# Performance work log

Hardware: AMD Instinct MI355X
Metric: run time of the kernel (lower is better)

Reference implementation:

```python
import jax, jax.numpy as jnp
import numpy as np

NUM_HEADS = 4
SPATIAL_DS = 2
EPS = 1e-5


def setup_inputs() -> dict:
    key = jax.random.key(0)
    ks = jax.random.split(key, 6)
    B, C, H, W = 8, 256, 64, 64
    hd = C // NUM_HEADS
    return {
        "x": jax.random.normal(ks[0], (B, C, H, W), jnp.float32),
        "gn_w": jnp.ones((C,), jnp.float32),
        "gn_b": jnp.zeros((C,), jnp.float32),
        "wq": jax.random.normal(ks[1], (C, C), jnp.float32) * (C ** -0.5),
        "wk": jax.random.normal(ks[2], (hd, C), jnp.float32) * (C ** -0.5),
        "wv": jax.random.normal(ks[3], (hd, C), jnp.float32) * (C ** -0.5),
        "wo": jax.random.normal(ks[4], (C, C), jnp.float32) * (C ** -0.5),
        "gamma": jnp.full((C,), 1e-4, jnp.float32),
    }


def reference(x, gn_w, gn_b, wq, wk, wv, wo, gamma):
    B, C, H, W = x.shape
    hd = C // NUM_HEADS
    scale = hd ** -0.5
    ds = SPATIAL_DS

    # GroupNorm with 1 group: normalize over (C,H,W) per sample, per-channel affine
    mu = jnp.mean(x, axis=(1, 2, 3), keepdims=True)
    var = jnp.var(x, axis=(1, 2, 3), keepdims=True)
    xn = (x - mu) * jax.lax.rsqrt(var + EPS)
    xn = xn * gn_w[None, :, None, None] + gn_b[None, :, None, None]

    # Q projection (1x1 conv == channel matmul): (B, heads, N, hd)
    q = jnp.einsum('oc,bchw->bohw', wq, xn).reshape(B, NUM_HEADS, hd, H * W)
    q = jnp.swapaxes(q, 2, 3)  # (B, h, N, hd)

    # AvgPool2d(ds, ds) on normalized input for K/V
    Hd, Wd = H // ds, W // ds
    x_ds = xn.reshape(B, C, Hd, ds, Wd, ds).mean(axis=(3, 5))

    k = jnp.einsum('oc,bchw->bohw', wk, x_ds).reshape(B, hd, Hd * Wd)
    k = jnp.swapaxes(k, 1, 2)  # (B, M, hd) single shared head
    v = jnp.einsum('oc,bchw->bohw', wv, x_ds).reshape(B, hd, Hd * Wd)
    v = jnp.swapaxes(v, 1, 2)  # (B, M, hd)

    # Multi-query attention: queries per-head, shared K/V
    attn = jnp.einsum('bhnd,bmd->bhnm', q, k) * scale
    attn = jax.nn.softmax(attn, axis=-1)
    out = jnp.einsum('bhnm,bmd->bhnd', attn, v)  # (B, h, N, hd)

    out = jnp.swapaxes(out, 2, 3).reshape(B, C, H, W)
    out = jnp.einsum('oc,bchw->bohw', wo, out)

    return x + out * gamma[None, :, None, None]
```

## Files before the change

### kernel.cpp

```cpp
#include <hip/hip_runtime.h>


#define CNT_INV (1.0f/1048576.0f)
#define EPSV 1e-5f
#define QSCALE 0.18033688f

#define WS_STATS 0
#define WS_XNT   64
#define WS_XDS   4194368
#define WS_K     5242944
#define WS_V     5505088
#define WS_WQB   5767232
#define WS_WKV   5800000
#define WS_WOB   5816384

typedef __attribute__((ext_vector_type(8))) short bf8_t;
typedef __attribute__((ext_vector_type(4))) float f4_t;

static __device__ __forceinline__ unsigned fbits(float f) {
  union { float f; unsigned u; } v; v.f = f; return v.u;
}
static __device__ __forceinline__ unsigned short f2bf(float f) {
  unsigned u = fbits(f);
  return (unsigned short)((u + 0x7fffu + ((u >> 16) & 1u)) >> 16);
}
static __device__ __forceinline__ unsigned pk_rnd(float a, float b) {
  return __builtin_amdgcn_perm(fbits(b) + 0x8000u, fbits(a) + 0x8000u, 0x07060302u);
}
static __device__ __forceinline__ unsigned pk_tr(float a, float b) {
  return __builtin_amdgcn_perm(fbits(b), fbits(a), 0x07060302u);
}
static __device__ __forceinline__ float bf2f(unsigned short h) {
  union { unsigned u; float f; } v; v.u = ((unsigned)h) << 16; return v.f;
}
static __device__ __forceinline__ float fexp2(float x) {
  float r; asm("v_exp_f32 %0, %1" : "=v"(r) : "v"(x)); return r;
}

__global__ __launch_bounds__(256) void k_prep_stats(const float* __restrict__ x,
                                                    const float* __restrict__ wq,
                                                    const float* __restrict__ wk,
                                                    const float* __restrict__ wv,
                                                    const float* __restrict__ wo,
                                                    float* __restrict__ stats,
                                                    unsigned short* __restrict__ wqb,
                                                    unsigned short* __restrict__ wkvb,
                                                    unsigned short* __restrict__ wob) {
  const int blk = blockIdx.x;
  const int t = threadIdx.x;
  if (blk < 512) {
    const int b = blk >> 6;
    const int chunk = blk & 63;
    const float4* xb = (const float4*)(x + (size_t)b * 1048576 + (size_t)chunk * 16384);
    float s = 0.f, s2 = 0.f;
#pragma unroll
    for (int it = 0; it < 16; ++it) {
      float4 v = xb[it * 256 + t];
      s  += v.x + v.y + v.z + v.w;
      s2 += v.x * v.x + v.y * v.y + v.z * v.z + v.w * v.w;
    }
#pragma unroll
    for (int o = 32; o > 0; o >>= 1) {
      s  += __shfl_down(s, o);
      s2 += __shfl_down(s2, o);
    }
    __shared__ float red[8];
    const int wid = t >> 6;
    if ((t & 63) == 0) { red[wid] = s; red[4 + wid] = s2; }
    __syncthreads();
    if (t == 0) {
      atomicAdd(&stats[b * 2 + 0], red[0] + red[1] + red[2] + red[3]);
      atomicAdd(&stats[b * 2 + 1], red[4] + red[5] + red[6] + red[7]);
    }
  } else {
    const int idx = (blk - 512) * 256 + t;
    if (idx < 65536) wqb[idx] = f2bf(wq[idx]);
    else if (idx < 81920) wkvb[idx - 65536] = f2bf(wk[idx - 65536]);
    else if (idx < 98304) wkvb[idx - 65536] = f2bf(wv[idx - 81920]);
    else if (idx < 163840) wob[idx - 98304] = f2bf(wo[idx - 98304]);
  }
}

__global__ __launch_bounds__(256) void k_xnt(const float* __restrict__ x,
                                             const float* __restrict__ gnw,
                                             const float* __restrict__ gnb,
                                             const float* __restrict__ stats,
                                             unsigned short* __restrict__ xnT,
                                             unsigned short* __restrict__ xdsT) {
  __shared__ unsigned short T[128][72];
  const int t = threadIdx.x;
  const int b = blockIdx.z, c0 = blockIdx.y * 64, hp = blockIdx.x;
  const int n0 = hp * 128;
  const float mu = stats[b * 2 + 0] * CNT_INV;
  const float rstd = rsqrtf(stats[b * 2 + 1] * CNT_INV - mu * mu + EPSV);
  const int n4 = (t & 31) * 4, cl = t >> 5;
#pragma unroll
  for (int p = 0; p < 8; ++p) {
    const int c = c0 + p * 8 + cl;
    const float gw = gnw[c] * rstd;
    const float gb = gnb[c] - mu * rstd * gnw[c];
    float4 v = *(const float4*)&x[(size_t)(b * 256 + c) * 4096 + n0 + n4];
    T[n4 + 0][p * 8 + cl] = f2bf(v.x * gw + gb);
    T[n4 + 1][p * 8 + cl] = f2bf(v.y * gw + gb);
    T[n4 + 2][p * 8 + cl] = f2bf(v.z * gw + gb);
    T[n4 + 3][p * 8 + cl] = f2bf(v.w * gw + gb);
  }
  __syncthreads();
  {
    const int r = t >> 1, ch = (t & 1) * 32;
    unsigned short* dst = xnT + ((size_t)b * 4096 + n0 + r) * 256 + c0 + ch;
#pragma unroll
    for (int u = 0; u < 4; ++u)
      *(uint4*)(dst + u * 8) = *(const uint4*)&T[r][ch + u * 8];
  }
  {
    const int wd = t >> 3, c8 = (t & 7) * 8;
    uint4 u0 = *(const uint4*)&T[2 * wd][c8];
    uint4 u1 = *(const uint4*)&T[2 * wd + 1][c8];
    uint4 u2 = *(const uint4*)&T[64 + 2 * wd][c8];
    uint4 u3 = *(const uint4*)&T[64 + 2 * wd + 1][c8];
    const unsigned* p0 = (const unsigned*)&u0; const unsigned* p1 = (const unsigned*)&u1;
    const unsigned* p2 = (const unsigned*)&u2; const unsigned* p3 = (const unsigned*)&u3;
    unsigned outp[4];
#pragma unroll
    for (int i = 0; i < 4; ++i) {
      float lo = (bf2f((unsigned short)p0[i]) + bf2f((unsigned short)p1[i]) +
                  bf2f((unsigned short)p2[i]) + bf2f((unsigned short)p3[i])) * 0.25f;
      float hi = (bf2f((unsigned short)(p0[i] >> 16)) + bf2f((unsigned short)(p1[i] >> 16)) +
                  bf2f((unsigned short)(p2[i] >> 16)) + bf2f((unsigned short)(p3[i] >> 16))) * 0.25f;
      outp[i] = pk_rnd(lo, hi);
    }
    *(uint4*)(xdsT + ((size_t)b * 1024 + hp * 32 + wd) * 256 + c0 + c8) = *(uint4*)outp;
  }
}

__global__ __launch_bounds__(256) void k_gemm_kv(const unsigned short* __restrict__ wkvb,
                                                 const unsigned short* __restrict__ xdsT,
                                                 unsigned short* __restrict__ kbf,
                                                 unsigned short* __restrict__ vtbf) {
  __shared__ __align__(16) unsigned short kv[2][64][72];
  const int t = threadIdx.x;
  const int w = t >> 6, l = t & 63, lane16 = l & 15, quad = l >> 4;
  const int m0 = blockIdx.x * 64, b = blockIdx.y;
  const unsigned short* Abase = wkvb + (size_t)(w * 32 + lane16) * 256 + quad * 8;
  const unsigned short* Bbase = xdsT + ((size_t)b * 1024 + m0 + lane16) * 256 + quad * 8;
  f4_t acc[2][4];
#pragma unroll
  for (int i = 0; i < 2; ++i)
#pragma unroll
    for (int j = 0; j < 4; ++j) acc[i][j] = (f4_t){0.f, 0.f, 0.f, 0.f};
  bf8_t Ac[2], Bc[4];
#pragma unroll
  for (int og = 0; og < 2; ++og) Ac[og] = *(const bf8_t*)(Abase + (size_t)og * 16 * 256);
#pragma unroll
  for (int mg = 0; mg < 4; ++mg) Bc[mg] = *(const bf8_t*)(Bbase + (size_t)mg * 16 * 256);
  for (int kc = 0; kc < 256; kc += 32) {
    const int kn = (kc + 32) & 255;
    bf8_t An[2], Bn[4];
#pragma unroll
    for (int og = 0; og < 2; ++og) An[og] = *(const bf8_t*)(Abase + (size_t)og * 16 * 256 + kn);
#pragma unroll
    for (int mg = 0; mg < 4; ++mg) Bn[mg] = *(const bf8_t*)(Bbase + (size_t)mg * 16 * 256 + kn);
#pragma unroll
    for (int og = 0; og < 2; ++og)
#pragma unroll
      for (int mg = 0; mg < 4; ++mg)
        acc[og][mg] = __builtin_amdgcn_mfma_f32_16x16x32_bf16(Ac[og], Bc[mg], acc[og][mg], 0, 0, 0);
#pragma unroll
    for (int og = 0; og < 2; ++og) Ac[og] = An[og];
#pragma unroll
    for (int mg = 0; mg < 4; ++mg) Bc[mg] = Bn[mg];
  }
  if (w < 2) {
#pragma unroll
    for (int og = 0; og < 2; ++og)
#pragma unroll
      for (int mg = 0; mg < 4; ++mg) {
        uint2 p;
        p.x = pk_rnd(acc[og][mg][0], acc[og][mg][1]);
        p.y = pk_rnd(acc[og][mg][2], acc[og][mg][3]);
        *(uint2*)&kv[0][mg * 16 + lane16][w * 32 + og * 16 + quad * 4] = p;
      }
  } else {
#pragma unroll
    for (int og = 0; og < 2; ++og)
#pragma unroll
      for (int mg = 0; mg < 4; ++mg) {
        const int d0 = (w - 2) * 32 + og * 16 + quad * 4;
#pragma unroll
        for (int r = 0; r < 4; ++r)
          kv[1][d0 + r][mg * 16 + lane16] = f2bf(acc[og][mg][r]);
      }
  }
  __syncthreads();
  {
    const int row = t >> 2, seg = (t & 3) * 16;
    uint4 k0 = *(const uint4*)&kv[0][row][seg];
    uint4 k1 = *(const uint4*)&kv[0][row][seg + 8];
    unsigned short* kd = kbf + (size_t)b * 65536 + (size_t)(m0 + row) * 64 + seg;
    *(uint4*)kd = k0; *(uint4*)(kd + 8) = k1;
    uint4 v0 = *(const uint4*)&kv[1][row][seg];
    uint4 v1 = *(const uint4*)&kv[1][row][seg + 8];
    unsigned short* vd = vtbf + (size_t)b * 65536 + (size_t)row * 1024 + m0 + seg;
    *(uint4*)vd = v0; *(uint4*)(vd + 8) = v1;
  }
}

__global__ __launch_bounds__(256) void k_fused(const unsigned short* __restrict__ wqb,
                                               const unsigned short* __restrict__ xnT,
                                               const unsigned short* __restrict__ kbf,
                                               const unsigned short* __restrict__ vtbf,
                                               const unsigned short* __restrict__ wob,
                                               const float* __restrict__ x,
                                               const float* __restrict__ gamma,
                                               float* __restrict__ outp) {
  __shared__ __align__(16) unsigned short smem[20480];
  const int t = threadIdx.x;
  const int w = t >> 6, l = t & 63, lane16 = l & 15, quad = l >> 4;
  const int n0 = blockIdx.x * 64, b = blockIdx.y;
  const int h = w;
  unsigned short* qst = smem + w * 4608;
  unsigned short (*plds)[64][40] = (unsigned short (*)[64][40])(smem + w * 5120);
  unsigned short (*aos)[264] = (unsigned short (*)[264])smem;

  const unsigned short* kb = kbf + (size_t)b * 65536;
  const unsigned short* vb = vtbf + (size_t)b * 65536;

  {
    const unsigned short* Abase = wqb + (size_t)(h * 64 + lane16) * 256 + quad * 8;
    const unsigned short* Bbase = xnT + ((size_t)b * 4096 + n0 + lane16) * 256 + quad * 8;
    f4_t qacc[4][4];
#pragma unroll
    for (int i = 0; i < 4; ++i)
#pragma unroll
      for (int j = 0; j < 4; ++j) qacc[i][j] = (f4_t){0.f, 0.f, 0.f, 0.f};
    for (int kc = 0; kc < 256; kc += 32) {
      bf8_t A[4], Bf[4];
#pragma unroll
      for (int og = 0; og < 4; ++og) A[og] = *(const bf8_t*)(Abase + (size_t)og * 16 * 256 + kc);
#pragma unroll
      for (int ng = 0; ng < 4; ++ng) Bf[ng] = *(const bf8_t*)(Bbase + (size_t)ng * 16 * 256 + kc);
#pragma unroll
      for (int og = 0; og < 4; ++og)
#pragma unroll
        for (int ng = 0; ng < 4; ++ng)
          qacc[og][ng] = __builtin_amdgcn_mfma_f32_16x16x32_bf16(A[og], Bf[ng], qacc[og][ng], 0, 0, 0);
    }
#pragma unroll
    for (int og = 0; og < 4; ++og)
#pragma unroll
      for (int ng = 0; ng < 4; ++ng) {
        uint2 p;
        p.x = pk_rnd(qacc[og][ng][0] * QSCALE, qacc[og][ng][1] * QSCALE);
        p.y = pk_rnd(qacc[og][ng][2] * QSCALE, qacc[og][ng][3] * QSCALE);
        *(uint2*)&qst[(ng * 16 + lane16) * 72 + og * 16 + quad * 4] = p;
      }
  }
  bf8_t Qf[4][2];
#pragma unroll
  for (int qg = 0; qg < 4; ++qg)
#pragma unroll
    for (int dc = 0; dc < 2; ++dc)
      Qf[qg][dc] = *(const bf8_t*)&qst[(qg * 16 + lane16) * 72 + dc * 32 + quad * 8];
  __syncthreads();

  f4_t O[4][4];
#pragma unroll
  for (int dg = 0; dg < 4; ++dg)
#pragma unroll
    for (int qg = 0; qg < 4; ++qg) O[dg][qg] = (f4_t){0.f, 0.f, 0.f, 0.f};
  f4_t O4[4];
#pragma unroll
  for (int qg = 0; qg < 4; ++qg) O4[qg] = (f4_t){0.f, 0.f, 0.f, 0.f};
  const short onebf = (lane16 == 0) ? (short)0x3F80 : (short)0;
  const bf8_t Aone = {onebf, onebf, onebf, onebf, onebf, onebf, onebf, onebf};

#define SSTEP(KREG, BUF)                                                      \
  {                                                                           \
    _Pragma("unroll")                                                         \
    for (int qg = 0; qg < 4; ++qg) {                                          \
      _Pragma("unroll")                                                       \
      for (int s = 0; s < 2; ++s) {                                           \
        f4_t S = (f4_t){0.f, 0.f, 0.f, 0.f};                                  \
        S = __builtin_amdgcn_mfma_f32_16x16x32_bf16(KREG[s][0], Qf[qg][0], S, 0, 0, 0); \
        S = __builtin_amdgcn_mfma_f32_16x16x32_bf16(KREG[s][1], Qf[qg][1], S, 0, 0, 0); \
        float e0 = fexp2(S[0]);                                               \
        float e1 = fexp2(S[1]);                                               \
        float e2 = fexp2(S[2]);                                               \
        float e3 = fexp2(S[3]);                                               \
        uint2 p; p.x = pk_tr(e0, e1); p.y = pk_tr(e2, e3);                    \
        *(uint2*)&plds[BUF][qg * 16 + lane16][s * 16 + quad * 4] = p;         \
      }                                                                       \
    }                                                                         \
  }

  bf8_t Kc[2][2];
#pragma unroll
  for (int s = 0; s < 2; ++s)
#pragma unroll
    for (int dc = 0; dc < 2; ++dc)
      Kc[s][dc] = *(const bf8_t*)(kb + (size_t)(s * 16 + lane16) * 64 + dc * 32 + quad * 8);
  SSTEP(Kc, 0);

  bf8_t Vc[4];
#pragma unroll
  for (int s = 0; s < 2; ++s)
#pragma unroll
    for (int dc = 0; dc < 2; ++dc)
      Kc[s][dc] = *(const bf8_t*)(kb + (size_t)(32 + s * 16 + lane16) * 64 + dc * 32 + quad * 8);
#pragma unroll
  for (int dg = 0; dg < 4; ++dg)
    Vc[dg] = *(const bf8_t*)(vb + (size_t)(dg * 16 + lane16) * 1024 + quad * 8);

  for (int it = 1; it < 32; ++it) {
    const int cb = it & 1, pb = cb ^ 1;
    bf8_t Pf[4];
#pragma unroll
    for (int qg = 0; qg < 4; ++qg)
      Pf[qg] = *(const bf8_t*)&plds[pb][qg * 16 + lane16][quad * 8];
    const int kvk = ((it + 1) & 31) * 32;
    const int kvv = it * 32;
    bf8_t K2[2][2], V2[4];
#pragma unroll
    for (int s = 0; s < 2; ++s)
#pragma unroll
      for (int dc = 0; dc < 2; ++dc)
        K2[s][dc] = *(const bf8_t*)(kb + (size_t)(kvk + s * 16 + lane16) * 64 + dc * 32 + quad * 8);
#pragma unroll
    for (int dg = 0; dg < 4; ++dg)
      V2[dg] = *(const bf8_t*)(vb + (size_t)(dg * 16 + lane16) * 1024 + kvv + quad * 8);
    __builtin_amdgcn_s_setprio(1);
#pragma unroll
    for (int dg = 0; dg < 4; ++dg)
#pragma unroll
      for (int qg = 0; qg < 4; ++qg)
        O[dg][qg] = __builtin_amdgcn_mfma_f32_16x16x32_bf16(Vc[dg], Pf[qg], O[dg][qg], 0, 0, 0);
#pragma unroll
    for (int qg = 0; qg < 4; ++qg)
      O4[qg] = __builtin_amdgcn_mfma_f32_16x16x32_bf16(Aone, Pf[qg], O4[qg], 0, 0, 0);
    __builtin_amdgcn_s_setprio(0);
    SSTEP(Kc, cb);
#pragma unroll
    for (int s = 0; s < 2; ++s)
#pragma unroll
      for (int dc = 0; dc < 2; ++dc) Kc[s][dc] = K2[s][dc];
#pragma unroll
    for (int dg = 0; dg < 4; ++dg) Vc[dg] = V2[dg];
  }
  {
    bf8_t Pf[4];
#pragma unroll
    for (int qg = 0; qg < 4; ++qg)
      Pf[qg] = *(const bf8_t*)&plds[1][qg * 16 + lane16][quad * 8];
    __builtin_amdgcn_s_setprio(1);
#pragma unroll
    for (int dg = 0; dg < 4; ++dg)
#pragma unroll
      for (int qg = 0; qg < 4; ++qg)
        O[dg][qg] = __builtin_amdgcn_mfma_f32_16x16x32_bf16(Vc[dg], Pf[qg], O[dg][qg], 0, 0, 0);
#pragma unroll
    for (int qg = 0; qg < 4; ++qg)
      O4[qg] = __builtin_amdgcn_mfma_f32_16x16x32_bf16(Aone, Pf[qg], O4[qg], 0, 0, 0);
    __builtin_amdgcn_s_setprio(0);
  }
#undef SSTEP

  float rden[4];
#pragma unroll
  for (int qg = 0; qg < 4; ++qg) {
    float d = __shfl(O4[qg][0], lane16);
    rden[qg] = 1.f / d;
  }

  __syncthreads();
#pragma unroll
  for (int dg = 0; dg < 4; ++dg)
#pragma unroll
    for (int qg = 0; qg < 4; ++qg) {
      const int c0 = h * 64 + dg * 16 + quad * 4;
      uint2 p;
      p.x = pk_rnd(O[dg][qg][0] * rden[qg], O[dg][qg][1] * rden[qg]);
      p.y = pk_rnd(O[dg][qg][2] * rden[qg], O[dg][qg][3] * rden[qg]);
      *(uint2*)&aos[qg * 16 + lane16][c0] = p;
    }
  __syncthreads();

  {
    const unsigned short* Wbase = wob + (size_t)(w * 64 + lane16) * 256 + quad * 8;
    f4_t acc[4][4];
#pragma unroll
    for (int i = 0; i < 4; ++i)
#pragma unroll
      for (int j = 0; j < 4; ++j) acc[i][j] = (f4_t){0.f, 0.f, 0.f, 0.f};
    for (int kc = 0; kc < 256; kc += 32) {
      bf8_t A[4], Bf[4];
#pragma unroll
      for (int og = 0; og < 4; ++og) A[og] = *(const bf8_t*)(Wbase + (size_t)og * 16 * 256 + kc);
#pragma unroll
      for (int ng = 0; ng < 4; ++ng) Bf[ng] = *(const bf8_t*)&aos[ng * 16 + lane16][kc + quad * 8];
#pragma unroll
      for (int og = 0; og < 4; ++og)
#pragma unroll
        for (int ng = 0; ng < 4; ++ng)
          acc[og][ng] = __builtin_amdgcn_mfma_f32_16x16x32_bf16(A[og], Bf[ng], acc[og][ng], 0, 0, 0);
    }
#pragma unroll
    for (int og = 0; og < 4; ++og) {
      float4 g4 = *(const float4*)&gamma[w * 64 + og * 16 + quad * 4];
      const float g[4] = {g4.x, g4.y, g4.z, g4.w};
#pragma unroll
      for (int ng = 0; ng < 4; ++ng) {
        const int n = n0 + ng * 16 + lane16;
#pragma unroll
        for (int r = 0; r < 4; ++r) {
          const int o = w * 64 + og * 16 + quad * 4 + r;
          const size_t ix = ((size_t)(b * 256 + o)) * 4096 + n;
          outp[ix] = x[ix] + g[r] * acc[og][ng][r];
        }
      }
    }
  }
}

extern "C" void kernel_launch(void* const* d_in, const int* in_sizes, int n_in,
                              void* d_out, int out_size, void* d_ws, size_t ws_size,
                              hipStream_t stream) {
  const float* x     = (const float*)d_in[0];
  const float* gnw   = (const float*)d_in[1];
  const float* gnb   = (const float*)d_in[2];
  const float* wq    = (const float*)d_in[3];
  const float* wk    = (const float*)d_in[4];
  const float* wv    = (const float*)d_in[5];
  const float* wo    = (const float*)d_in[6];
  const float* gamma = (const float*)d_in[7];
  float* out = (float*)d_out;
  float* ws  = (float*)d_ws;
  unsigned short* xnT  = (unsigned short*)(ws + WS_XNT);
  unsigned short* xdsT = (unsigned short*)(ws + WS_XDS);
  unsigned short* kbf  = (unsigned short*)(ws + WS_K);
  unsigned short* vtbf = (unsigned short*)(ws + WS_V);
  unsigned short* wqb  = (unsigned short*)(ws + WS_WQB);
  unsigned short* wkvb = (unsigned short*)(ws + WS_WKV);
  unsigned short* wob  = (unsigned short*)(ws + WS_WOB);

  hipMemsetAsync(ws, 0, 256, stream);
  k_prep_stats<<<1152, 256, 0, stream>>>(x, wq, wk, wv, wo, ws + WS_STATS, wqb, wkvb, wob);
  k_xnt<<<dim3(32, 4, 8), 256, 0, stream>>>(x, gnw, gnb, ws + WS_STATS, xnT, xdsT);
  k_gemm_kv<<<dim3(16, 8), 256, 0, stream>>>(wkvb, xdsT, kbf, vtbf);
  k_fused<<<dim3(64, 8), 256, 0, stream>>>(wqb, xnT, kbf, vtbf, wob, x, gamma, out);
}
```

Baseline: 217.4 us.

## Keep attention probabilities in registers via 16x16x16 MFMA and swizzle transpose LDS

The attention loop now feeds the exp'd scores straight from the QK^T accumulator layout into PV MFMAs using 16x16x16 bf16 instructions with matching 4-element V fragments. This removes the per-wave LDS round trip and double buffer for P, and drops one __syncthreads. The trade is twice as many smaller MFMAs for the PV product and loss of the old software pipeline that overlapped PV of one tile with QK of the next. Separately, the GroupNorm transpose kernel XOR-swizzles its shared tile columns to cut LDS bank conflicts on its writes and reads.

```diff
diff --git a/kernel.cpp b/kernel.cpp
--- a/kernel.cpp
+++ b/kernel.cpp
@@ -15,6 +15,7 @@
 #define WS_WOB   5816384
 
 typedef __attribute__((ext_vector_type(8))) short bf8_t;
+typedef __attribute__((ext_vector_type(4))) short bf4_t;
 typedef __attribute__((ext_vector_type(4))) float f4_t;
 
 static __device__ __forceinline__ unsigned fbits(float f) {
@@ -35,6 +36,12 @@
 }
 static __device__ __forceinline__ float fexp2(float x) {
   float r; asm("v_exp_f32 %0, %1" : "=v"(r) : "v"(x)); return r;
+}
+static __device__ __forceinline__ bf4_t pk2(float a, float b, float c, float d) {
+  union { unsigned u[2]; bf4_t v; } pu;
+  pu.u[0] = pk_tr(a, b);
+  pu.u[1] = pk_tr(c, d);
+  return pu.v;
 }
 
 __global__ __launch_bounds__(256) void k_prep_stats(const float* __restrict__ x,
@@ -94,31 +101,36 @@
   const float mu = stats[b * 2 + 0] * CNT_INV;
   const float rstd = rsqrtf(stats[b * 2 + 1] * CNT_INV - mu * mu + EPSV);
   const int n4 = (t & 31) * 4, cl = t >> 5;
+  const int wswz = t & 7;
 #pragma unroll
   for (int p = 0; p < 8; ++p) {
     const int c = c0 + p * 8 + cl;
     const float gw = gnw[c] * rstd;
     const float gb = gnb[c] - mu * rstd * gnw[c];
+    const int pc = (p ^ wswz) * 8 + cl;
     float4 v = *(const float4*)&x[(size_t)(b * 256 + c) * 4096 + n0 + n4];
-    T[n4 + 0][p * 8 + cl] = f2bf(v.x * gw + gb);
-    T[n4 + 1][p * 8 + cl] = f2bf(v.y * gw + gb);
-    T[n4 + 2][p * 8 + cl] = f2bf(v.z * gw + gb);
-    T[n4 + 3][p * 8 + cl] = f2bf(v.w * gw + gb);
+    T[n4 + 0][pc] = f2bf(v.x * gw + gb);
+    T[n4 + 1][pc] = f2bf(v.y * gw + gb);
+    T[n4 + 2][pc] = f2bf(v.z * gw + gb);
+    T[n4 + 3][pc] = f2bf(v.w * gw + gb);
   }
   __syncthreads();
   {
-    const int r = t >> 1, ch = (t & 1) * 32;
-    unsigned short* dst = xnT + ((size_t)b * 4096 + n0 + r) * 256 + c0 + ch;
+    const int r = t >> 1, cb4 = (t & 1) * 4;
+    const int rswz = (t >> 3) & 7;
+    unsigned short* dst = xnT + ((size_t)b * 4096 + n0 + r) * 256 + c0 + cb4 * 8;
 #pragma unroll
     for (int u = 0; u < 4; ++u)
-      *(uint4*)(dst + u * 8) = *(const uint4*)&T[r][ch + u * 8];
+      *(uint4*)(dst + u * 8) = *(const uint4*)&T[r][((cb4 + u) ^ rswz) * 8];
   }
   {
-    const int wd = t >> 3, c8 = (t & 7) * 8;
-    uint4 u0 = *(const uint4*)&T[2 * wd][c8];
-    uint4 u1 = *(const uint4*)&T[2 * wd + 1][c8];
-    uint4 u2 = *(const uint4*)&T[64 + 2 * wd][c8];
-    uint4 u3 = *(const uint4*)&T[64 + 2 * wd + 1][c8];
+    const int wd = t >> 3, c8 = t & 7;
+    const int pswz = (wd >> 1) & 7;
+    const int pc = (c8 ^ pswz) * 8;
+    uint4 u0 = *(const uint4*)&T[2 * wd][pc];
+    uint4 u1 = *(const uint4*)&T[2 * wd + 1][pc];
+    uint4 u2 = *(const uint4*)&T[64 + 2 * wd][pc];
+    uint4 u3 = *(const uint4*)&T[64 + 2 * wd + 1][pc];
     const unsigned* p0 = (const unsigned*)&u0; const unsigned* p1 = (const unsigned*)&u1;
     const unsigned* p2 = (const unsigned*)&u2; const unsigned* p3 = (const unsigned*)&u3;
     unsigned outp[4];
@@ -130,7 +142,7 @@
                   bf2f((unsigned short)(p2[i] >> 16)) + bf2f((unsigned short)(p3[i] >> 16))) * 0.25f;
       outp[i] = pk_rnd(lo, hi);
     }
-    *(uint4*)(xdsT + ((size_t)b * 1024 + hp * 32 + wd) * 256 + c0 + c8) = *(uint4*)outp;
+    *(uint4*)(xdsT + ((size_t)b * 1024 + hp * 32 + wd) * 256 + c0 + c8 * 8) = *(uint4*)outp;
   }
 }
 
@@ -214,13 +226,12 @@
                                                const float* __restrict__ x,
                                                const float* __restrict__ gamma,
                                                float* __restrict__ outp) {
-  __shared__ __align__(16) unsigned short smem[20480];
+  __shared__ __align__(16) unsigned short smem[18432];
   const int t = threadIdx.x;
   const int w = t >> 6, l = t & 63, lane16 = l & 15, quad = l >> 4;
   const int n0 = blockIdx.x * 64, b = blockIdx.y;
   const int h = w;
   unsigned short* qst = smem + w * 4608;
-  unsigned short (*plds)[64][40] = (unsigned short (*)[64][40])(smem + w * 5120);
   unsigned short (*aos)[264] = (unsigned short (*)[264])smem;
 
   const unsigned short* kb = kbf + (size_t)b * 65536;
@@ -273,97 +284,65 @@
 #pragma unroll
   for (int qg = 0; qg < 4; ++qg) O4[qg] = (f4_t){0.f, 0.f, 0.f, 0.f};
   const short onebf = (lane16 == 0) ? (short)0x3F80 : (short)0;
-  const bf8_t Aone = {onebf, onebf, onebf, onebf, onebf, onebf, onebf, onebf};
-
-#define SSTEP(KREG, BUF)                                                      \
-  {                                                                           \
-    _Pragma("unroll")                                                         \
-    for (int qg = 0; qg < 4; ++qg) {                                          \
-      _Pragma("unroll")                                                       \
-      for (int s = 0; s < 2; ++s) {                                           \
-        f4_t S = (f4_t){0.f, 0.f, 0.f, 0.f};                                  \
-        S = __builtin_amdgcn_mfma_f32_16x16x32_bf16(KREG[s][0], Qf[qg][0], S, 0, 0, 0); \
-        S = __builtin_amdgcn_mfma_f32_16x16x32_bf16(KREG[s][1], Qf[qg][1], S, 0, 0, 0); \
-        float e0 = fexp2(S[0]);                                               \
-        float e1 = fexp2(S[1]);                                               \
-        float e2 = fexp2(S[2]);                                               \
-        float e3 = fexp2(S[3]);                                               \
-        uint2 p; p.x = pk_tr(e0, e1); p.y = pk_tr(e2, e3);                    \
-        *(uint2*)&plds[BUF][qg * 16 + lane16][s * 16 + quad * 4] = p;         \
-      }                                                                       \
-    }                                                                         \
-  }
+  const bf4_t Aone = {onebf, onebf, onebf, onebf};
 
   bf8_t Kc[2][2];
+  bf4_t Va[4][2];
 #pragma unroll
   for (int s = 0; s < 2; ++s)
 #pragma unroll
     for (int dc = 0; dc < 2; ++dc)
       Kc[s][dc] = *(const bf8_t*)(kb + (size_t)(s * 16 + lane16) * 64 + dc * 32 + quad * 8);
-  SSTEP(Kc, 0);
-
-  bf8_t Vc[4];
-#pragma unroll
-  for (int s = 0; s < 2; ++s)
-#pragma unroll
-    for (int dc = 0; dc < 2; ++dc)
-      Kc[s][dc] = *(const bf8_t*)(kb + (size_t)(32 + s * 16 + lane16) * 64 + dc * 32 + quad * 8);
 #pragma unroll
   for (int dg = 0; dg < 4; ++dg)
-    Vc[dg] = *(const bf8_t*)(vb + (size_t)(dg * 16 + lane16) * 1024 + quad * 8);
-
-  for (int it = 1; it < 32; ++it) {
-    const int cb = it & 1, pb = cb ^ 1;
-    bf8_t Pf[4];
-#pragma unroll
-    for (int qg = 0; qg < 4; ++qg)
-      Pf[qg] = *(const bf8_t*)&plds[pb][qg * 16 + lane16][quad * 8];
-    const int kvk = ((it + 1) & 31) * 32;
-    const int kvv = it * 32;
-    bf8_t K2[2][2], V2[4];
 #pragma unroll
     for (int s = 0; s < 2; ++s)
+      Va[dg][s] = *(const bf4_t*)(vb + (size_t)(dg * 16 + lane16) * 1024 + s * 16 + quad * 4);
+
+  for (int it = 0; it < 32; ++it) {
+    const int kvn = ((it + 1) & 31) * 32;
+    bf8_t K2[2][2];
+    bf4_t V2[4][2];
+#pragma unroll
+    for (int s = 0; s < 2; ++s)
 #pragma unroll
       for (int dc = 0; dc < 2; ++dc)
-        K2[s][dc] = *(const bf8_t*)(kb + (size_t)(kvk + s * 16 + lane16) * 64 + dc * 32 + quad * 8);
+        K2[s][dc] = *(const bf8_t*)(kb + (size_t)(kvn + s * 16 + lane16) * 64 + dc * 32 + quad * 8);
 #pragma unroll
     for (int dg = 0; dg < 4; ++dg)
-      V2[dg] = *(const bf8_t*)(vb + (size_t)(dg * 16 + lane16) * 1024 + kvv + quad * 8);
-    __builtin_amdgcn_s_setprio(1);
+#pragma unroll
+      for (int s = 0; s < 2; ++s)
+        V2[dg][s] = *(const bf4_t*)(vb + (size_t)(dg * 16 + lane16) * 1024 + kvn + s * 16 + quad * 4);
+
+#pragma unroll
+    for (int qg = 0; qg < 4; ++qg) {
+      f4_t S0 = (f4_t){0.f, 0.f, 0.f, 0.f};
+      f4_t S1 = (f4_t){0.f, 0.f, 0.f, 0.f};
+      S0 = __builtin_amdgcn_mfma_f32_16x16x32_bf16(Kc[0][0], Qf[qg][0], S0, 0, 0, 0);
+      S0 = __builtin_amdgcn_mfma_f32_16x16x32_bf16(Kc[0][1], Qf[qg][1], S0, 0, 0, 0);
+      S1 = __builtin_amdgcn_mfma_f32_16x16x32_bf16(Kc[1][0], Qf[qg][0], S1, 0, 0, 0);
+      S1 = __builtin_amdgcn_mfma_f32_16x16x32_bf16(Kc[1][1], Qf[qg][1], S1, 0, 0, 0);
+      bf4_t P0 = pk2(fexp2(S0[0]), fexp2(S0[1]), fexp2(S0[2]), fexp2(S0[3]));
+      bf4_t P1 = pk2(fexp2(S1[0]), fexp2(S1[1]), fexp2(S1[2]), fexp2(S1[3]));
+      __builtin_amdgcn_s_setprio(1);
+#pragma unroll
+      for (int dg = 0; dg < 4; ++dg) {
+        O[dg][qg] = __builtin_amdgcn_mfma_f32_16x16x16bf16_1k(Va[dg][0], P0, O[dg][qg], 0, 0, 0);
+        O[dg][qg] = __builtin_amdgcn_mfma_f32_16x16x16bf16_1k(Va[dg][1], P1, O[dg][qg], 0, 0, 0);
+      }
+      O4[qg] = __builtin_amdgcn_mfma_f32_16x16x16bf16_1k(Aone, P0, O4[qg], 0, 0, 0);
+      O4[qg] = __builtin_amdgcn_mfma_f32_16x16x16bf16_1k(Aone, P1, O4[qg], 0, 0, 0);
+      __builtin_amdgcn_s_setprio(0);
+    }
+#pragma unroll
+    for (int s = 0; s < 2; ++s)
+#pragma unroll
+      for (int dc = 0; dc < 2; ++dc) Kc[s][dc] = K2[s][dc];
 #pragma unroll
     for (int dg = 0; dg < 4; ++dg)
 #pragma unroll
-      for (int qg = 0; qg < 4; ++qg)
-        O[dg][qg] = __builtin_amdgcn_mfma_f32_16x16x32_bf16(Vc[dg], Pf[qg], O[dg][qg], 0, 0, 0);
-#pragma unroll
-    for (int qg = 0; qg < 4; ++qg)
-      O4[qg] = __builtin_amdgcn_mfma_f32_16x16x32_bf16(Aone, Pf[qg], O4[qg], 0, 0, 0);
-    __builtin_amdgcn_s_setprio(0);
-    SSTEP(Kc, cb);
-#pragma unroll
-    for (int s = 0; s < 2; ++s)
-#pragma unroll
-      for (int dc = 0; dc < 2; ++dc) Kc[s][dc] = K2[s][dc];
-#pragma unroll
-    for (int dg = 0; dg < 4; ++dg) Vc[dg] = V2[dg];
-  }
-  {
-    bf8_t Pf[4];
-#pragma unroll
-    for (int qg = 0; qg < 4; ++qg)
-      Pf[qg] = *(const bf8_t*)&plds[1][qg * 16 + lane16][quad * 8];
-    __builtin_amdgcn_s_setprio(1);
-#pragma unroll
-    for (int dg = 0; dg < 4; ++dg)
-#pragma unroll
-      for (int qg = 0; qg < 4; ++qg)
-        O[dg][qg] = __builtin_amdgcn_mfma_f32_16x16x32_bf16(Vc[dg], Pf[qg], O[dg][qg], 0, 0, 0);
-#pragma unroll
-    for (int qg = 0; qg < 4; ++qg)
-      O4[qg] = __builtin_amdgcn_mfma_f32_16x16x32_bf16(Aone, Pf[qg], O4[qg], 0, 0, 0);
-    __builtin_amdgcn_s_setprio(0);
-  }
-#undef SSTEP
+      for (int s = 0; s < 2; ++s) Va[dg][s] = V2[dg][s];
+  }
 
   float rden[4];
 #pragma unroll
@@ -372,7 +351,6 @@
     rden[qg] = 1.f / d;
   }
 
-  __syncthreads();
 #pragma unroll
   for (int dg = 0; dg < 4; ++dg)
 #pragma unroll
```

Result: slower. 242.4 us (+11.5%).

## Stage K/V tiles through shared LDS with swizzled layouts in fused attention

Applied to the files above, without the earlier changes.

The fused attention kernel stops loading K and V fragments straight from global memory in every wave. Instead, the block cooperatively stages each 32-row K/V window into double-buffered LDS, issuing the next window's global load early, and each wave then reads its fragments from LDS. The K/V producer kernel now writes K with an XOR swizzle and V in window-blocked order so the staging copies are contiguous. XOR swizzles are also added to the LDS transpose in the normalize kernel to reduce bank conflicts. The cost is an extra block-wide barrier per iteration and more LDS use.

```diff
diff --git a/kernel.cpp b/kernel.cpp
--- a/kernel.cpp
+++ b/kernel.cpp
@@ -94,31 +94,36 @@
   const float mu = stats[b * 2 + 0] * CNT_INV;
   const float rstd = rsqrtf(stats[b * 2 + 1] * CNT_INV - mu * mu + EPSV);
   const int n4 = (t & 31) * 4, cl = t >> 5;
+  const int wswz = t & 7;
 #pragma unroll
   for (int p = 0; p < 8; ++p) {
     const int c = c0 + p * 8 + cl;
     const float gw = gnw[c] * rstd;
     const float gb = gnb[c] - mu * rstd * gnw[c];
+    const int pc = (p ^ wswz) * 8 + cl;
     float4 v = *(const float4*)&x[(size_t)(b * 256 + c) * 4096 + n0 + n4];
-    T[n4 + 0][p * 8 + cl] = f2bf(v.x * gw + gb);
-    T[n4 + 1][p * 8 + cl] = f2bf(v.y * gw + gb);
-    T[n4 + 2][p * 8 + cl] = f2bf(v.z * gw + gb);
-    T[n4 + 3][p * 8 + cl] = f2bf(v.w * gw + gb);
-  }
-  __syncthreads();
-  {
-    const int r = t >> 1, ch = (t & 1) * 32;
-    unsigned short* dst = xnT + ((size_t)b * 4096 + n0 + r) * 256 + c0 + ch;
+    T[n4 + 0][pc] = f2bf(v.x * gw + gb);
+    T[n4 + 1][pc] = f2bf(v.y * gw + gb);
+    T[n4 + 2][pc] = f2bf(v.z * gw + gb);
+    T[n4 + 3][pc] = f2bf(v.w * gw + gb);
+  }
+  __syncthreads();
+  {
+    const int r = t >> 1, cb4 = (t & 1) * 4;
+    const int rswz = (t >> 3) & 7;
+    unsigned short* dst = xnT + ((size_t)b * 4096 + n0 + r) * 256 + c0 + cb4 * 8;
 #pragma unroll
     for (int u = 0; u < 4; ++u)
-      *(uint4*)(dst + u * 8) = *(const uint4*)&T[r][ch + u * 8];
-  }
-  {
-    const int wd = t >> 3, c8 = (t & 7) * 8;
-    uint4 u0 = *(const uint4*)&T[2 * wd][c8];
-    uint4 u1 = *(const uint4*)&T[2 * wd + 1][c8];
-    uint4 u2 = *(const uint4*)&T[64 + 2 * wd][c8];
-    uint4 u3 = *(const uint4*)&T[64 + 2 * wd + 1][c8];
+      *(uint4*)(dst + u * 8) = *(const uint4*)&T[r][((cb4 + u) ^ rswz) * 8];
+  }
+  {
+    const int wd = t >> 3, c8 = t & 7;
+    const int pswz = (wd >> 1) & 7;
+    const int pc = (c8 ^ pswz) * 8;
+    uint4 u0 = *(const uint4*)&T[2 * wd][pc];
+    uint4 u1 = *(const uint4*)&T[2 * wd + 1][pc];
+    uint4 u2 = *(const uint4*)&T[64 + 2 * wd][pc];
+    uint4 u3 = *(const uint4*)&T[64 + 2 * wd + 1][pc];
     const unsigned* p0 = (const unsigned*)&u0; const unsigned* p1 = (const unsigned*)&u1;
     const unsigned* p2 = (const unsigned*)&u2; const unsigned* p3 = (const unsigned*)&u3;
     unsigned outp[4];
@@ -130,7 +135,7 @@
                   bf2f((unsigned short)(p2[i] >> 16)) + bf2f((unsigned short)(p3[i] >> 16))) * 0.25f;
       outp[i] = pk_rnd(lo, hi);
     }
-    *(uint4*)(xdsT + ((size_t)b * 1024 + hp * 32 + wd) * 256 + c0 + c8) = *(uint4*)outp;
+    *(uint4*)(xdsT + ((size_t)b * 1024 + hp * 32 + wd) * 256 + c0 + c8 * 8) = *(uint4*)outp;
   }
 }
 
@@ -194,14 +199,17 @@
   }
   __syncthreads();
   {
-    const int row = t >> 2, seg = (t & 3) * 16;
-    uint4 k0 = *(const uint4*)&kv[0][row][seg];
-    uint4 k1 = *(const uint4*)&kv[0][row][seg + 8];
-    unsigned short* kd = kbf + (size_t)b * 65536 + (size_t)(m0 + row) * 64 + seg;
-    *(uint4*)kd = k0; *(uint4*)(kd + 8) = k1;
-    uint4 v0 = *(const uint4*)&kv[1][row][seg];
-    uint4 v1 = *(const uint4*)&kv[1][row][seg + 8];
-    unsigned short* vd = vtbf + (size_t)b * 65536 + (size_t)row * 1024 + m0 + seg;
+    const int row = t >> 2, q2 = t & 3;
+    const int e = row & 7;
+    uint4 k0 = *(const uint4*)&kv[0][row][q2 * 16];
+    uint4 k1 = *(const uint4*)&kv[0][row][q2 * 16 + 8];
+    unsigned short* kd = kbf + (size_t)b * 65536 + (size_t)(m0 + row) * 64;
+    *(uint4*)(kd + ((q2 * 2) ^ e) * 8)     = k0;
+    *(uint4*)(kd + ((q2 * 2 + 1) ^ e) * 8) = k1;
+    uint4 v0 = *(const uint4*)&kv[1][row][q2 * 16];
+    uint4 v1 = *(const uint4*)&kv[1][row][q2 * 16 + 8];
+    unsigned short* vd = vtbf + (size_t)b * 65536 + (size_t)(blockIdx.x * 2 + (q2 >> 1)) * 2048 +
+                         (size_t)row * 32 + (q2 & 1) * 16;
     *(uint4*)vd = v0; *(uint4*)(vd + 8) = v1;
   }
 }
@@ -215,6 +223,8 @@
                                                const float* __restrict__ gamma,
                                                float* __restrict__ outp) {
   __shared__ __align__(16) unsigned short smem[20480];
+  __shared__ __align__(16) unsigned short kst[2][2048];
+  __shared__ __align__(16) unsigned short vst[2][2048];
   const int t = threadIdx.x;
   const int w = t >> 6, l = t & 63, lane16 = l & 15, quad = l >> 4;
   const int n0 = blockIdx.x * 64, b = blockIdx.y;
@@ -223,8 +233,35 @@
   unsigned short (*plds)[64][40] = (unsigned short (*)[64][40])(smem + w * 5120);
   unsigned short (*aos)[264] = (unsigned short (*)[264])smem;
 
-  const unsigned short* kb = kbf + (size_t)b * 65536;
-  const unsigned short* vb = vtbf + (size_t)b * 65536;
+  const int sw = w & 1;
+  const unsigned short* sbase = (w < 2) ? (kbf + (size_t)b * 65536) : (vtbf + (size_t)b * 65536);
+  unsigned short* sdst0 = ((w < 2) ? &kst[0][0] : &vst[0][0]) + sw * 1024 + l * 8;
+  unsigned short* sdst1 = ((w < 2) ? &kst[1][0] : &vst[1][0]) + sw * 1024 + l * 8;
+
+#define STAGE_ISSUE(WIN, R0, R1)                                              \
+  { const unsigned short* sp = sbase + (size_t)(WIN) * 2048 + sw * 1024 + l * 8; \
+    R0 = *(const uint4*)sp; R1 = *(const uint4*)(sp + 512); }
+#define STAGE_WRITE(DP, R0, R1)                                               \
+  { *(uint4*)(DP) = R0; *(uint4*)((DP) + 512) = R1; }
+
+#define READ_K(BUF, KREG)                                                     \
+  {                                                                           \
+    _Pragma("unroll")                                                         \
+    for (int s = 0; s < 2; ++s) {                                             \
+      _Pragma("unroll")                                                       \
+      for (int dc = 0; dc < 2; ++dc)                                          \
+        KREG[s][dc] = *(const bf8_t*)&kst[BUF][(s * 16 + lane16) * 64 +       \
+                                              (((dc * 4 + quad) ^ (lane16 & 7)) * 8)]; \
+    }                                                                         \
+  }
+#define READ_V(BUF, VREG)                                                     \
+  {                                                                           \
+    _Pragma("unroll")                                                         \
+    for (int dg = 0; dg < 4; ++dg)                                            \
+      VREG[dg] = *(const bf8_t*)&vst[BUF][(dg * 16 + lane16) * 32 + quad * 8]; \
+  }
+
+  const unsigned short* kb = kbf;
 
   {
     const unsigned short* Abase = wqb + (size_t)(h * 64 + lane16) * 256 + quad * 8;
@@ -294,41 +331,32 @@
     }                                                                         \
   }
 
-  bf8_t Kc[2][2];
-#pragma unroll
-  for (int s = 0; s < 2; ++s)
-#pragma unroll
-    for (int dc = 0; dc < 2; ++dc)
-      Kc[s][dc] = *(const bf8_t*)(kb + (size_t)(s * 16 + lane16) * 64 + dc * 32 + quad * 8);
+  {
+    uint4 a0, a1, b0, b1;
+    STAGE_ISSUE(0, a0, a1);
+    STAGE_ISSUE(1, b0, b1);
+    STAGE_WRITE(sdst0, a0, a1);
+    STAGE_WRITE(sdst1, b0, b1);
+  }
+  __syncthreads();
+
+  bf8_t Kc[2][2], Vc[4];
+  READ_K(0, Kc);
   SSTEP(Kc, 0);
-
-  bf8_t Vc[4];
-#pragma unroll
-  for (int s = 0; s < 2; ++s)
-#pragma unroll
-    for (int dc = 0; dc < 2; ++dc)
-      Kc[s][dc] = *(const bf8_t*)(kb + (size_t)(32 + s * 16 + lane16) * 64 + dc * 32 + quad * 8);
-#pragma unroll
-  for (int dg = 0; dg < 4; ++dg)
-    Vc[dg] = *(const bf8_t*)(vb + (size_t)(dg * 16 + lane16) * 1024 + quad * 8);
+  READ_V(0, Vc);
+  __syncthreads();
 
   for (int it = 1; it < 32; ++it) {
-    const int cb = it & 1, pb = cb ^ 1;
+    const int cur = it & 1, pb = cur ^ 1;
+    uint4 g0, g1;
+    if (it < 31) STAGE_ISSUE(it + 1, g0, g1);
     bf8_t Pf[4];
 #pragma unroll
     for (int qg = 0; qg < 4; ++qg)
       Pf[qg] = *(const bf8_t*)&plds[pb][qg * 16 + lane16][quad * 8];
-    const int kvk = ((it + 1) & 31) * 32;
-    const int kvv = it * 32;
-    bf8_t K2[2][2], V2[4];
-#pragma unroll
-    for (int s = 0; s < 2; ++s)
-#pragma unroll
-      for (int dc = 0; dc < 2; ++dc)
-        K2[s][dc] = *(const bf8_t*)(kb + (size_t)(kvk + s * 16 + lane16) * 64 + dc * 32 + quad * 8);
-#pragma unroll
-    for (int dg = 0; dg < 4; ++dg)
-      V2[dg] = *(const bf8_t*)(vb + (size_t)(dg * 16 + lane16) * 1024 + kvv + quad * 8);
+    READ_K(cur, Kc);
+    bf8_t Vn[4];
+    READ_V(cur, Vn);
     __builtin_amdgcn_s_setprio(1);
 #pragma unroll
     for (int dg = 0; dg < 4; ++dg)
@@ -339,13 +367,11 @@
     for (int qg = 0; qg < 4; ++qg)
       O4[qg] = __builtin_amdgcn_mfma_f32_16x16x32_bf16(Aone, Pf[qg], O4[qg], 0, 0, 0);
     __builtin_amdgcn_s_setprio(0);
-    SSTEP(Kc, cb);
-#pragma unroll
-    for (int s = 0; s < 2; ++s)
-#pragma unroll
-      for (int dc = 0; dc < 2; ++dc) Kc[s][dc] = K2[s][dc];
-#pragma unroll
-    for (int dg = 0; dg < 4; ++dg) Vc[dg] = V2[dg];
+    SSTEP(Kc, cur);
+#pragma unroll
+    for (int dg = 0; dg < 4; ++dg) Vc[dg] = Vn[dg];
+    if (it < 31) STAGE_WRITE((cur ? sdst0 : sdst1), g0, g1);
+    __syncthreads();
   }
   {
     bf8_t Pf[4];
@@ -364,6 +390,11 @@
     __builtin_amdgcn_s_setprio(0);
   }
 #undef SSTEP
+#undef STAGE_ISSUE
+#undef STAGE_WRITE
+#undef READ_K
+#undef READ_V
+  (void)kb;
 
   float rden[4];
 #pragma unroll
```

Measured after the change: 194.1 us. -10.7%, faster.
